# Performance work log

Measured on AMD Instinct MI355X. Metric: run time of the kernel, lower is better.

Reference implementation:

```python
import jax, jax.numpy as jnp
import numpy as np

TOP_K = 2


def setup_inputs() -> dict:
    key = jax.random.key(0)
    kx, kw = jax.random.split(key)
    x = jax.random.normal(kx, (4, 4096, 2048), dtype=jnp.float32)
    router_weights = jax.random.normal(kw, (8, 2048), dtype=jnp.float32) * 0.02
    return {"x": x, "router_weights": router_weights}


def reference(x, router_weights):
    # logits[b,s,e] = sum_d x[b,s,d] * W[e,d]
    logits = jnp.einsum('bsd,ed->bse', x, router_weights)
    # top-k over experts, then softmax over the selected k logits
    top_vals, top_idx = jax.lax.top_k(logits, TOP_K)  # [B,S,K]
    gates = jax.nn.softmax(top_vals, axis=-1)
    indices = top_idx.astype(jnp.int32)
    return indices, gates, logits
```

## Files before the change

### kernel.cpp

```cpp
#include <hip/hip_runtime.h>
#include <math.h>


constexpr int D      = 2048;
constexpr int E      = 8;
constexpr int T      = 4;
constexpr int WAVES  = 4;
constexpr int TOKENS = 16384;

typedef float f32x4 __attribute__((ext_vector_type(4)));

__device__ __forceinline__ bool better(float va, int ia, float vb, int ib) {
    return (va > vb) || (va == vb && ia < ib);
}

__global__ __launch_bounds__(256, 4)
void moe_router_kernel(const float* __restrict__ x,
                       const float* __restrict__ w,
                       float* __restrict__ out)
{
    const int lane = threadIdx.x & 63;
    const int wave = threadIdx.x >> 6;
    const int tok0 = (blockIdx.x * WAVES + wave) * T;

    float acc[T * E];
#pragma unroll
    for (int i = 0; i < T * E; ++i) acc[i] = 0.0f;

#pragma unroll 4
    for (int it = 0; it < D / 256; ++it) {
        const int d = it * 256 + lane * 4;
        f32x4 xv[T];
#pragma unroll
        for (int t = 0; t < T; ++t)
            xv[t] = *reinterpret_cast<const f32x4*>(x + (size_t)(tok0 + t) * D + d);
#pragma unroll
        for (int e = 0; e < E; ++e) {
            const f32x4 wv = *reinterpret_cast<const f32x4*>(w + e * D + d);
#pragma unroll
            for (int t = 0; t < T; ++t) {
                float a = acc[t * E + e];
                a = fmaf(xv[t].x, wv.x, a);
                a = fmaf(xv[t].y, wv.y, a);
                a = fmaf(xv[t].z, wv.z, a);
                a = fmaf(xv[t].w, wv.w, a);
                acc[t * E + e] = a;
            }
        }
    }

#pragma unroll
    for (int i = 0; i < 32; ++i) acc[i] += __shfl_xor(acc[i], 32, 64);

    const bool s16 = (lane & 16) != 0;
    float r16[16];
#pragma unroll
    for (int i = 0; i < 16; ++i) {
        const float keep = s16 ? acc[i + 16] : acc[i];
        const float send = s16 ? acc[i]      : acc[i + 16];
        r16[i] = keep + __shfl_xor(send, 16, 64);
    }
    const bool s8 = (lane & 8) != 0;
    float r8[8];
#pragma unroll
    for (int i = 0; i < 8; ++i) {
        const float keep = s8 ? r16[i + 8] : r16[i];
        const float send = s8 ? r16[i]     : r16[i + 8];
        r8[i] = keep + __shfl_xor(send, 8, 64);
    }
    const bool s4 = (lane & 4) != 0;
    float r4[4];
#pragma unroll
    for (int i = 0; i < 4; ++i) {
        const float keep = s4 ? r8[i + 4] : r8[i];
        const float send = s4 ? r8[i]     : r8[i + 4];
        r4[i] = keep + __shfl_xor(send, 4, 64);
    }
    const bool s2 = (lane & 2) != 0;
    float r2[2];
#pragma unroll
    for (int i = 0; i < 2; ++i) {
        const float keep = s2 ? r4[i + 2] : r4[i];
        const float send = s2 ? r4[i]     : r4[i + 2];
        r2[i] = keep + __shfl_xor(send, 2, 64);
    }
    const bool s1 = (lane & 1) != 0;
    float logit;
    {
        const float keep = s1 ? r2[1] : r2[0];
        const float send = s1 ? r2[0] : r2[1];
        logit = keep + __shfl_xor(send, 1, 64);
    }

    const int  e      = lane & 7;
    const int  t      = (lane >> 3) & 3;
    const int  token  = tok0 + t;
    const bool writer = lane < 32;

    float* out_idx    = out;
    float* out_gate   = out + TOKENS * 2;
    float* out_logits = out + TOKENS * 4;

    if (writer) out_logits[(size_t)tok0 * E + lane] = logit;

    float v1 = logit, v2 = -INFINITY;
    int   i1 = e,     i2 = E;
#pragma unroll
    for (int m = 1; m <= 4; m <<= 1) {
        float ov1 = __shfl_xor(v1, m, 64);
        int   oi1 = __shfl_xor(i1, m, 64);
        float ov2 = __shfl_xor(v2, m, 64);
        int   oi2 = __shfl_xor(i2, m, 64);
        float nv1, nv2; int ni1, ni2;
        if (better(v1, i1, ov1, oi1)) {
            nv1 = v1; ni1 = i1;
            if (better(v2, i2, ov1, oi1)) { nv2 = v2;  ni2 = i2;  }
            else                          { nv2 = ov1; ni2 = oi1; }
        } else {
            nv1 = ov1; ni1 = oi1;
            if (better(ov2, oi2, v1, i1)) { nv2 = ov2; ni2 = oi2; }
            else                          { nv2 = v1;  ni2 = i1;  }
        }
        v1 = nv1; i1 = ni1; v2 = nv2; i2 = ni2;
    }

    if (writer && e < 2) {
        const float ed  = expf(v2 - v1);
        const float inv = 1.0f / (1.0f + ed);
        const float g   = (e == 0) ? inv : ed * inv;
        out_idx [token * 2 + e] = (float)((e == 0) ? i1 : i2);
        out_gate[token * 2 + e] = g;
    }
}

extern "C" void kernel_launch(void* const* d_in, const int* in_sizes, int n_in,
                              void* d_out, int out_size, void* d_ws, size_t ws_size,
                              hipStream_t stream) {
    const float* x = (const float*)d_in[0];
    const float* w = (const float*)d_in[1];
    float* out = (float*)d_out;
    hipLaunchKernelGGL(moe_router_kernel, dim3(1024), dim3(256), 0, stream,
                       x, w, out);
}
```

Measured before the change: 194.7 us.

## Split D across wave pairs with 8 tokens per wave and LDS combine

Each wave now handles 8 tokens instead of 4, and each pair of waves splits the hidden dimension in half. The two partial logits are combined through shared memory after a block barrier. Loading more tokens per weight load halves how often the router weights are reloaded, while the reduction network gains a 32-lane stage that uses all 64 lanes. The cost is 64 accumulators per thread, which raises register pressure and may lower occupancy, plus a __syncthreads and an unroll-1 loop that exposes less memory-level parallelism.

Result: slower. 210.2 us (+8.0%).

```diff
diff --git a/kernel.cpp b/kernel.cpp
--- a/kernel.cpp
+++ b/kernel.cpp
@@ -4,8 +4,7 @@
 
 constexpr int D      = 2048;
 constexpr int E      = 8;
-constexpr int T      = 4;
-constexpr int WAVES  = 4;
+constexpr int T      = 8;
 constexpr int TOKENS = 16384;
 
 typedef float f32x4 __attribute__((ext_vector_type(4)));
@@ -20,23 +19,28 @@
                        float* __restrict__ out)
 {
     const int lane = threadIdx.x & 63;
-    const int wave = threadIdx.x >> 6;
-    const int tok0 = (blockIdx.x * WAVES + wave) * T;
+    const int wid  = threadIdx.x >> 6;
+    const int pair = wid >> 1;
+    const int half = wid & 1;
+    const int tok0 = (blockIdx.x * 2 + pair) * T;
+
+    const float* xbase = x + (size_t)tok0 * D + half * (D / 2) + lane * 4;
+    const float* wbase = w + half * (D / 2) + lane * 4;
 
     float acc[T * E];
 #pragma unroll
     for (int i = 0; i < T * E; ++i) acc[i] = 0.0f;
 
-#pragma unroll 4
-    for (int it = 0; it < D / 256; ++it) {
-        const int d = it * 256 + lane * 4;
+#pragma unroll 1
+    for (int it = 0; it < D / 512; ++it) {
+        const int d = it * 256;
         f32x4 xv[T];
 #pragma unroll
         for (int t = 0; t < T; ++t)
-            xv[t] = *reinterpret_cast<const f32x4*>(x + (size_t)(tok0 + t) * D + d);
+            xv[t] = *reinterpret_cast<const f32x4*>(xbase + (size_t)t * D + d);
 #pragma unroll
         for (int e = 0; e < E; ++e) {
-            const f32x4 wv = *reinterpret_cast<const f32x4*>(w + e * D + d);
+            const f32x4 wv = *reinterpret_cast<const f32x4*>(wbase + e * D + d);
 #pragma unroll
             for (int t = 0; t < T; ++t) {
                 float a = acc[t * E + e];
@@ -49,15 +53,20 @@
         }
     }
 
+    const bool s32 = (lane & 32) != 0;
+    float r32[32];
 #pragma unroll
-    for (int i = 0; i < 32; ++i) acc[i] += __shfl_xor(acc[i], 32, 64);
-
+    for (int i = 0; i < 32; ++i) {
+        const float keep = s32 ? acc[i + 32] : acc[i];
+        const float send = s32 ? acc[i]      : acc[i + 32];
+        r32[i] = keep + __shfl_xor(send, 32, 64);
+    }
     const bool s16 = (lane & 16) != 0;
     float r16[16];
 #pragma unroll
     for (int i = 0; i < 16; ++i) {
-        const float keep = s16 ? acc[i + 16] : acc[i];
-        const float send = s16 ? acc[i]      : acc[i + 16];
+        const float keep = s16 ? r32[i + 16] : r32[i];
+        const float send = s16 ? r32[i]      : r32[i + 16];
         r16[i] = keep + __shfl_xor(send, 16, 64);
     }
     const bool s8 = (lane & 8) != 0;
@@ -85,23 +94,27 @@
         r2[i] = keep + __shfl_xor(send, 2, 64);
     }
     const bool s1 = (lane & 1) != 0;
-    float logit;
+    float partial;
     {
         const float keep = s1 ? r2[1] : r2[0];
         const float send = s1 ? r2[0] : r2[1];
-        logit = keep + __shfl_xor(send, 1, 64);
+        partial = keep + __shfl_xor(send, 1, 64);
     }
 
-    const int  e      = lane & 7;
-    const int  t      = (lane >> 3) & 3;
-    const int  token  = tok0 + t;
-    const bool writer = lane < 32;
+    __shared__ float part[2][2][64];
+    part[pair][half][lane] = partial;
+    __syncthreads();
+    const float logit = part[pair][0][lane] + part[pair][1][lane];
+
+    const int e     = lane & 7;
+    const int t     = lane >> 3;
+    const int token = tok0 + t;
 
     float* out_idx    = out;
     float* out_gate   = out + TOKENS * 2;
     float* out_logits = out + TOKENS * 4;
 
-    if (writer) out_logits[(size_t)tok0 * E + lane] = logit;
+    if (half == 0) out_logits[(size_t)tok0 * E + lane] = logit;
 
     float v1 = logit, v2 = -INFINITY;
     int   i1 = e,     i2 = E;
@@ -124,7 +137,7 @@
         v1 = nv1; i1 = ni1; v2 = nv2; i2 = ni2;
     }
 
-    if (writer && e < 2) {
+    if (half == 0 && e < 2) {
         const float ed  = expf(v2 - v1);
         const float inv = 1.0f / (1.0f + ed);
         const float g   = (e == 0) ? inv : ed * inv;
```
